# Kernel tuning notes

Measured on AMD Instinct MI355X. Metric: run time of the kernel, lower is better.

## Reference

```python
import jax, jax.numpy as jnp
import numpy as np


def setup_inputs() -> dict:
    key = jax.random.key(0)
    kq, kk, kv = jax.random.split(key, 3)
    B, H, S, D = 4, 16, 1024, 64
    Q = jax.random.normal(kq, (B, H, S, D), dtype=jnp.float32)
    K = jax.random.normal(kk, (B, H, S, D), dtype=jnp.float32)
    V = jax.random.normal(kv, (B, H, S, D), dtype=jnp.float32)
    attn_mask = jnp.ones((B, 1, 1, S), dtype=jnp.int32)  # unused by the original forward
    return {"Q": Q, "K": K, "V": V, "attn_mask": attn_mask, "d_k": D}


def reference(Q, K, V, attn_mask, d_k):
    # scores = Q @ K^T / sqrt(d_k)   -> [B, H, S, S]
    scores = jnp.einsum("bhqd,bhkd->bhqk", Q, K) / jnp.sqrt(jnp.float32(d_k))
    # attn_mask is accepted but never applied in the original module.
    p_attn = jax.nn.softmax(scores, axis=-1)
    out = jnp.einsum("bhqk,bhkd->bhqd", p_attn, V)  # [B, H, S, D]
    return (out, p_attn)
```

## Files before the change

kernel.cpp:

```cpp
#include <hip/hip_runtime.h>
#include <hip/hip_bf16.h>

#define B_N 4
#define H_N 16
#define S_N 1024
#define D_N 64
#define NELEM (B_N * H_N * S_N * D_N)

typedef __bf16 bf16;
typedef bf16  bf16x4 __attribute__((ext_vector_type(4)));
typedef bf16  bf16x8 __attribute__((ext_vector_type(8)));
typedef float f32x4  __attribute__((ext_vector_type(4)));
typedef unsigned int u32x2 __attribute__((ext_vector_type(2)));

#define AS1 __attribute__((address_space(1)))
#define AS3 __attribute__((address_space(3)))
#define GLL16(gp, lp) __builtin_amdgcn_global_load_lds((const AS1 void*)(gp), (AS3 void*)(lp), 16, 0, 0)

__global__ __launch_bounds__(256)
void prep_kv(const float* __restrict__ K, const float* __restrict__ V,
             bf16* __restrict__ Kb, bf16* __restrict__ Vt)
{
    const int b = blockIdx.x;
    if (b < 2048) {
        int t = b * 256 + threadIdx.x;
        int row = t >> 3, sub = t & 7;
        const float* src = K + (size_t)row * 64 + sub * 8;
        float4 f0 = *(const float4*)src;
        float4 f1 = *(const float4*)(src + 4);
        bf16x8 o;
        o[0] = (bf16)f0.x; o[1] = (bf16)f0.y; o[2] = (bf16)f0.z; o[3] = (bf16)f0.w;
        o[4] = (bf16)f1.x; o[5] = (bf16)f1.y; o[6] = (bf16)f1.z; o[7] = (bf16)f1.w;
        int slot = sub ^ (row & 7);
        *(bf16x8*)(Kb + (size_t)row * 64 + slot * 8) = o;
    } else {
        int wid  = (b - 2048) * 4 + (threadIdx.x >> 6);
        int lane = threadIdx.x & 63;
        int bh = wid >> 7, chunk = wid & 127;
        const float* src = V + (size_t)bh * S_N * D_N + (size_t)chunk * 8 * 64 + lane;
        bf16x8 o;
#pragma unroll
        for (int j = 0; j < 8; ++j) o[j] = (bf16)src[j * 64];
        int slot = (chunk & 7) ^ (lane & 7);
        bf16* dst = Vt + (size_t)bh * D_N * S_N + (size_t)lane * S_N
                       + (chunk >> 3) * 64 + slot * 8;
        *(bf16x8*)dst = o;
    }
}

__global__ __launch_bounds__(256)
void sdpa_main(const float* __restrict__ Qf, const bf16* __restrict__ Kb,
               const bf16* __restrict__ Vt, float* __restrict__ Og,
               float* __restrict__ Pg)
{
    __shared__ __attribute__((aligned(128))) bf16 K_lds[2][4096];
    __shared__ __attribute__((aligned(128))) bf16 V_lds[2][4096];
    __shared__ __attribute__((aligned(128))) bf16 Pt_lds[4][1024];

    const int bid = blockIdx.x;
    const int swz = (bid & 7) * 128 + (bid >> 3);
    const int bh = swz >> 4, qtile = swz & 15;

    const int tid = threadIdx.x;
    const int wave = tid >> 6, lane = tid & 63;
    const int l16 = lane & 15, lgrp = lane >> 4;
    const int swx = (l16 & 7) << 4;

    const float* Qp = Qf + (size_t)bh * S_N * D_N;
    const bf16* Kp = Kb + (size_t)bh * S_N * D_N;
    const bf16* Vp = Vt + (size_t)bh * D_N * S_N;
    float* Op = Og + (size_t)bh * S_N * D_N;
    float* Pp = Pg + (size_t)bh * S_N * S_N;

    const int qrow = qtile * 64 + wave * 16 + l16;
    bf16x8 aq[2];
#pragma unroll
    for (int ds = 0; ds < 2; ++ds) {
        const float* src = Qp + (size_t)qrow * 64 + ds * 32 + lgrp * 8;
        float4 f0 = *(const float4*)src;
        float4 f1 = *(const float4*)(src + 4);
        aq[ds][0] = (bf16)(f0.x * 0.125f); aq[ds][1] = (bf16)(f0.y * 0.125f);
        aq[ds][2] = (bf16)(f0.z * 0.125f); aq[ds][3] = (bf16)(f0.w * 0.125f);
        aq[ds][4] = (bf16)(f1.x * 0.125f); aq[ds][5] = (bf16)(f1.y * 0.125f);
        aq[ds][6] = (bf16)(f1.z * 0.125f); aq[ds][7] = (bf16)(f1.w * 0.125f);
    }

    auto stage_k = [&](int kt, bf16* dst) {
        const bf16* gk = Kp + (size_t)kt * 64;
        GLL16(gk + (wave    ) * 512 + lane * 8, dst + (wave    ) * 512);
        GLL16(gk + (wave + 4) * 512 + lane * 8, dst + (wave + 4) * 512);
    };
    auto stage_k2 = [&](int kt, bf16* dst0, bf16* dst1) {
        const bf16* gk = Kp + (size_t)kt * 64;
        GLL16(gk + (wave     ) * 512 + lane * 8, dst0 + (wave    ) * 512);
        GLL16(gk + (wave + 4 ) * 512 + lane * 8, dst0 + (wave + 4) * 512);
        GLL16(gk + (wave + 8 ) * 512 + lane * 8, dst1 + (wave    ) * 512);
        GLL16(gk + (wave + 12) * 512 + lane * 8, dst1 + (wave + 4) * 512);
    };
    auto stage_v = [&](int kt, bf16* dst) {
        const int dr = lane >> 3, c7 = lane & 7;
        GLL16(Vp + (size_t)((wave    ) * 8 + dr) * S_N + kt + c7 * 8, dst + (wave    ) * 512);
        GLL16(Vp + (size_t)((wave + 4) * 8 + dr) * S_N + kt + c7 * 8, dst + (wave + 4) * 512);
    };

    auto scores = [&](const bf16* base, f32x4 (&acc)[4]) {
#pragma unroll
        for (int kb = 0; kb < 4; ++kb) {
            acc[kb] = (f32x4){0.f, 0.f, 0.f, 0.f};
#pragma unroll
            for (int ds = 0; ds < 2; ++ds) {
                bf16x8 bk = *(const bf16x8*)((const char*)base
                            + (kb * 16 + l16) * 128
                            + ((ds * 64 + lgrp * 16) ^ swx));
                acc[kb] = __builtin_amdgcn_mfma_f32_16x16x32_bf16(aq[ds], bk, acc[kb], 0, 0, 0);
            }
        }
    };

    float lsum[4] = {0.f, 0.f, 0.f, 0.f};
    stage_k2(0, &K_lds[0][0], &K_lds[1][0]);
    __syncthreads();
    for (int c = 0; c < 8; ++c) {
        const bf16* b0 = (c & 1) ? &V_lds[0][0] : &K_lds[0][0];
        const bf16* b1 = (c & 1) ? &V_lds[1][0] : &K_lds[1][0];
        bf16* n0 = (c & 1) ? &K_lds[0][0] : &V_lds[0][0];
        bf16* n1 = (c & 1) ? &K_lds[1][0] : &V_lds[1][0];
        if (c < 7) stage_k2((c + 1) * 128, n0, n1);
        f32x4 acc[4];
        scores(b0, acc);
#pragma unroll
        for (int kb = 0; kb < 4; ++kb)
#pragma unroll
            for (int r = 0; r < 4; ++r) lsum[r] += __expf(acc[kb][r]);
        scores(b1, acc);
#pragma unroll
        for (int kb = 0; kb < 4; ++kb)
#pragma unroll
            for (int r = 0; r < 4; ++r) lsum[r] += __expf(acc[kb][r]);
        __syncthreads();
    }
    float rl[4];
#pragma unroll
    for (int r = 0; r < 4; ++r) {
        float s = lsum[r];
        s += __shfl_xor(s, 1, 64);
        s += __shfl_xor(s, 2, 64);
        s += __shfl_xor(s, 4, 64);
        s += __shfl_xor(s, 8, 64);
        rl[r] = 1.0f / s;
    }

    f32x4 oacc[4];
#pragma unroll
    for (int db = 0; db < 4; ++db) oacc[db] = (f32x4){0.f, 0.f, 0.f, 0.f};

    const unsigned ptoff = (unsigned)(uintptr_t)(AS3 bf16*)(&Pt_lds[wave][0]);
    const int qg = qtile * 64 + wave * 16 + l16;

    stage_k(0, &K_lds[0][0]);
    stage_v(0, &V_lds[0][0]);
    __syncthreads();
    for (int t = 0; t < 16; ++t) {
        const int kt = t * 64, buf = t & 1;

        f32x4 acc[4];
        scores(&K_lds[buf][0], acc);

        if (t < 15) {
            stage_k(kt + 64, &K_lds[buf ^ 1][0]);
            stage_v(kt + 64, &V_lds[buf ^ 1][0]);
        }

#pragma unroll
        for (int kb = 0; kb < 4; ++kb) {
            bf16x4 pk;
#pragma unroll
            for (int r = 0; r < 4; ++r) pk[r] = (bf16)(__expf(acc[kb][r]) * rl[r]);
            *(bf16x4*)((char*)&Pt_lds[wave][0] + (kb * 16 + l16) * 32 + lgrp * 8) = pk;
        }
        asm volatile("s_waitcnt lgkmcnt(0)" ::: "memory");

        const bf16* vb = &V_lds[buf][0];
#pragma unroll
        for (int ks = 0; ks < 2; ++ks) {
            bf16x8 bv0 = *(const bf16x8*)((const char*)vb + (l16     ) * 128 + ((ks * 64 + lgrp * 16) ^ swx));
            bf16x8 bv1 = *(const bf16x8*)((const char*)vb + (16 + l16) * 128 + ((ks * 64 + lgrp * 16) ^ swx));
            bf16x8 bv2 = *(const bf16x8*)((const char*)vb + (32 + l16) * 128 + ((ks * 64 + lgrp * 16) ^ swx));
            bf16x8 bv3 = *(const bf16x8*)((const char*)vb + (48 + l16) * 128 + ((ks * 64 + lgrp * 16) ^ swx));

            u32x2 t0, t1;
            unsigned a = ptoff + ks * 1024 + lgrp * 256 + l16 * 8;
            asm volatile("ds_read_b64_tr_b16 %0, %2\n\t"
                         "ds_read_b64_tr_b16 %1, %2 offset:128"
                         : "=&v"(t0), "=&v"(t1) : "v"(a));
            asm volatile("s_waitcnt lgkmcnt(0)" ::: "memory");
            __builtin_amdgcn_sched_barrier(0);

            bf16x8 ap;
            ((unsigned*)&ap)[0] = t0[0]; ((unsigned*)&ap)[1] = t0[1];
            ((unsigned*)&ap)[2] = t1[0]; ((unsigned*)&ap)[3] = t1[1];

            float4 o0, o1;
            o0.x = __uint_as_float(t0[0] << 16);
            o0.y = __uint_as_float(t0[0] & 0xffff0000u);
            o0.z = __uint_as_float(t0[1] << 16);
            o0.w = __uint_as_float(t0[1] & 0xffff0000u);
            o1.x = __uint_as_float(t1[0] << 16);
            o1.y = __uint_as_float(t1[0] & 0xffff0000u);
            o1.z = __uint_as_float(t1[1] << 16);
            o1.w = __uint_as_float(t1[1] & 0xffff0000u);
            float* pp = Pp + (size_t)qg * S_N + kt + ks * 32 + lgrp * 8;
            *(float4*)pp = o0;
            *(float4*)(pp + 4) = o1;

            oacc[0] = __builtin_amdgcn_mfma_f32_16x16x32_bf16(ap, bv0, oacc[0], 0, 0, 0);
            oacc[1] = __builtin_amdgcn_mfma_f32_16x16x32_bf16(ap, bv1, oacc[1], 0, 0, 0);
            oacc[2] = __builtin_amdgcn_mfma_f32_16x16x32_bf16(ap, bv2, oacc[2], 0, 0, 0);
            oacc[3] = __builtin_amdgcn_mfma_f32_16x16x32_bf16(ap, bv3, oacc[3], 0, 0, 0);
        }
        __syncthreads();
    }

    const int qb0 = qtile * 64 + wave * 16 + lgrp * 4;
#pragma unroll
    for (int db = 0; db < 4; ++db)
#pragma unroll
        for (int r = 0; r < 4; ++r)
            Op[(size_t)(qb0 + r) * D_N + db * 16 + l16] = oacc[db][r];
}

__global__ __launch_bounds__(256)
void sdpa_fused(const float* __restrict__ Qg, const float* __restrict__ Kg,
                const float* __restrict__ Vg, float* __restrict__ Og,
                float* __restrict__ Pg)
{
    constexpr int LDP = 72;
    __shared__ bf16 K_lds [64][LDP];
    __shared__ bf16 Vt_lds[64][LDP];
    __shared__ bf16 P_lds [4][16][LDP];

    const int qtile = blockIdx.x;
    const int bh    = blockIdx.y;
    const int tid   = threadIdx.x;
    const int wave  = tid >> 6;
    const int lane  = tid & 63;
    const int l16   = lane & 15;
    const int lgrp  = lane >> 4;

    const float* Qp = Qg + (size_t)bh * S_N * D_N;
    const float* Kp = Kg + (size_t)bh * S_N * D_N;
    const float* Vp = Vg + (size_t)bh * S_N * D_N;
    float* Op = Og + (size_t)bh * S_N * D_N;
    float* Pp = Pg + (size_t)bh * S_N * S_N;

    const int qrow = qtile * 64 + wave * 16 + l16;
    bf16x8 aq[2];
#pragma unroll
    for (int ds = 0; ds < 2; ++ds) {
        const float* src = Qp + qrow * D_N + ds * 32 + lgrp * 8;
        float4 f0 = *(const float4*)(src);
        float4 f1 = *(const float4*)(src + 4);
        aq[ds][0] = (bf16)(f0.x * 0.125f); aq[ds][1] = (bf16)(f0.y * 0.125f);
        aq[ds][2] = (bf16)(f0.z * 0.125f); aq[ds][3] = (bf16)(f0.w * 0.125f);
        aq[ds][4] = (bf16)(f1.x * 0.125f); aq[ds][5] = (bf16)(f1.y * 0.125f);
        aq[ds][6] = (bf16)(f1.z * 0.125f); aq[ds][7] = (bf16)(f1.w * 0.125f);
    }

    auto stage_k = [&](int kt) {
#pragma unroll
        for (int i = 0; i < 4; ++i) {
            int slot = tid + i * 256;
            int row = slot >> 4, c4 = slot & 15;
            float4 f = *(const float4*)(Kp + (kt + row) * D_N + c4 * 4);
            bf16x4 pk = {(bf16)f.x, (bf16)f.y, (bf16)f.z, (bf16)f.w};
            *(bf16x4*)&K_lds[row][c4 * 4] = pk;
        }
    };
    auto stage_v = [&](int kt) {
#pragma unroll
        for (int i = 0; i < 4; ++i) {
            int slot = tid + i * 256;
            int row = slot >> 4, c4 = slot & 15;
            float4 f = *(const float4*)(Vp + (kt + row) * D_N + c4 * 4);
            Vt_lds[c4 * 4 + 0][row] = (bf16)f.x;
            Vt_lds[c4 * 4 + 1][row] = (bf16)f.y;
            Vt_lds[c4 * 4 + 2][row] = (bf16)f.z;
            Vt_lds[c4 * 4 + 3][row] = (bf16)f.w;
        }
    };
    auto compute_scores = [&](f32x4 (&acc)[4]) {
#pragma unroll
        for (int kb = 0; kb < 4; ++kb) {
            acc[kb] = (f32x4){0.f, 0.f, 0.f, 0.f};
#pragma unroll
            for (int ds = 0; ds < 2; ++ds) {
                bf16x8 bk = *(const bf16x8*)&K_lds[kb * 16 + l16][ds * 32 + lgrp * 8];
                acc[kb] = __builtin_amdgcn_mfma_f32_16x16x32_bf16(aq[ds], bk, acc[kb], 0, 0, 0);
            }
        }
    };

    float lsum[4] = {0.f, 0.f, 0.f, 0.f};
    for (int kt = 0; kt < S_N; kt += 64) {
        __syncthreads();
        stage_k(kt);
        __syncthreads();
        f32x4 acc[4];
        compute_scores(acc);
#pragma unroll
        for (int kb = 0; kb < 4; ++kb)
#pragma unroll
            for (int r = 0; r < 4; ++r) lsum[r] += __expf(acc[kb][r]);
    }
    float rl[4];
#pragma unroll
    for (int r = 0; r < 4; ++r) {
        float s = lsum[r];
        s += __shfl_xor(s, 1, 64);
        s += __shfl_xor(s, 2, 64);
        s += __shfl_xor(s, 4, 64);
        s += __shfl_xor(s, 8, 64);
        rl[r] = 1.0f / s;
    }

    f32x4 oacc[4];
#pragma unroll
    for (int db = 0; db < 4; ++db) oacc[db] = (f32x4){0.f, 0.f, 0.f, 0.f};
    const int qb0 = qtile * 64 + wave * 16 + lgrp * 4;

    for (int kt = 0; kt < S_N; kt += 64) {
        __syncthreads();
        stage_k(kt);
        stage_v(kt);
        __syncthreads();

        f32x4 acc[4];
        compute_scores(acc);
#pragma unroll
        for (int kb = 0; kb < 4; ++kb) {
#pragma unroll
            for (int r = 0; r < 4; ++r) {
                float p = __expf(acc[kb][r]) * rl[r];
                Pp[(size_t)(qb0 + r) * S_N + (kt + kb * 16 + l16)] = p;
                P_lds[wave][lgrp * 4 + r][kb * 16 + l16] = (bf16)p;
            }
        }
#pragma unroll
        for (int ks = 0; ks < 2; ++ks) {
            bf16x8 ap = *(const bf16x8*)&P_lds[wave][l16][ks * 32 + lgrp * 8];
#pragma unroll
            for (int db = 0; db < 4; ++db) {
                bf16x8 bv = *(const bf16x8*)&Vt_lds[db * 16 + l16][ks * 32 + lgrp * 8];
                oacc[db] = __builtin_amdgcn_mfma_f32_16x16x32_bf16(ap, bv, oacc[db], 0, 0, 0);
            }
        }
    }

#pragma unroll
    for (int db = 0; db < 4; ++db)
#pragma unroll
        for (int r = 0; r < 4; ++r)
            Op[(size_t)(qb0 + r) * D_N + db * 16 + l16] = oacc[db][r];
}

extern "C" void kernel_launch(void* const* d_in, const int* in_sizes, int n_in,
                              void* d_out, int out_size, void* d_ws, size_t ws_size,
                              hipStream_t stream) {
    const float* Q = (const float*)d_in[0];
    const float* K = (const float*)d_in[1];
    const float* V = (const float*)d_in[2];
    float* Out = (float*)d_out;
    float* P   = (float*)d_out + (size_t)NELEM;

    const size_t need = (size_t)NELEM * 2 * 2;
    if (ws_size >= need) {
        bf16* Kb = (bf16*)d_ws;
        bf16* Vt = Kb + NELEM;
        prep_kv<<<dim3(4096), dim3(256), 0, stream>>>(K, V, Kb, Vt);
        sdpa_main<<<dim3(1024), dim3(256), 0, stream>>>(Q, Kb, Vt, Out, P);
    } else {
        sdpa_fused<<<dim3(16, 64), dim3(256), 0, stream>>>(Q, K, V, Out, P);
    }
}
```

Before: 96.24 us.

## Cache unnormalized bf16 exp scores in registers to skip second QK^T pass

The first pass now keeps exp(scores) as bf16 in a register array, 64 bf16x4 values per thread, while accumulating row sums. The second pass then only rescales these cached values and streams V, instead of recomputing QK^T and exp from K in LDS. This removes half the MFMA score work and the second round of K loads, but adds heavy register pressure that can lower occupancy or cause spills. It also adds double rounding to bf16 (exp, then normalized P), which changes precision slightly.

```diff
diff --git a/kernel.cpp b/kernel.cpp
--- a/kernel.cpp
+++ b/kernel.cpp
@@ -90,13 +90,6 @@
         GLL16(gk + (wave    ) * 512 + lane * 8, dst + (wave    ) * 512);
         GLL16(gk + (wave + 4) * 512 + lane * 8, dst + (wave + 4) * 512);
     };
-    auto stage_k2 = [&](int kt, bf16* dst0, bf16* dst1) {
-        const bf16* gk = Kp + (size_t)kt * 64;
-        GLL16(gk + (wave     ) * 512 + lane * 8, dst0 + (wave    ) * 512);
-        GLL16(gk + (wave + 4 ) * 512 + lane * 8, dst0 + (wave + 4) * 512);
-        GLL16(gk + (wave + 8 ) * 512 + lane * 8, dst1 + (wave    ) * 512);
-        GLL16(gk + (wave + 12) * 512 + lane * 8, dst1 + (wave + 4) * 512);
-    };
     auto stage_v = [&](int kt, bf16* dst) {
         const int dr = lane >> 3, c7 = lane & 7;
         GLL16(Vp + (size_t)((wave    ) * 8 + dr) * S_N + kt + c7 * 8, dst + (wave    ) * 512);
@@ -117,26 +110,29 @@
         }
     };
 
+    bf16x4 pc[16][4];
+
     float lsum[4] = {0.f, 0.f, 0.f, 0.f};
-    stage_k2(0, &K_lds[0][0], &K_lds[1][0]);
+    stage_k(0, &K_lds[0][0]);
     __syncthreads();
-    for (int c = 0; c < 8; ++c) {
-        const bf16* b0 = (c & 1) ? &V_lds[0][0] : &K_lds[0][0];
-        const bf16* b1 = (c & 1) ? &V_lds[1][0] : &K_lds[1][0];
-        bf16* n0 = (c & 1) ? &K_lds[0][0] : &V_lds[0][0];
-        bf16* n1 = (c & 1) ? &K_lds[1][0] : &V_lds[1][0];
-        if (c < 7) stage_k2((c + 1) * 128, n0, n1);
+#pragma unroll
+    for (int t = 0; t < 16; ++t) {
+        const int buf = t & 1;
+        if (t < 15) stage_k((t + 1) * 64, &K_lds[buf ^ 1][0]);
+        if (t == 15) stage_v(0, &V_lds[0][0]);
         f32x4 acc[4];
-        scores(b0, acc);
-#pragma unroll
-        for (int kb = 0; kb < 4; ++kb)
-#pragma unroll
-            for (int r = 0; r < 4; ++r) lsum[r] += __expf(acc[kb][r]);
-        scores(b1, acc);
-#pragma unroll
-        for (int kb = 0; kb < 4; ++kb)
-#pragma unroll
-            for (int r = 0; r < 4; ++r) lsum[r] += __expf(acc[kb][r]);
+        scores(&K_lds[buf][0], acc);
+#pragma unroll
+        for (int kb = 0; kb < 4; ++kb) {
+            bf16x4 pk;
+#pragma unroll
+            for (int r = 0; r < 4; ++r) {
+                float e = __expf(acc[kb][r]);
+                lsum[r] += e;
+                pk[r] = (bf16)e;
+            }
+            pc[t][kb] = pk;
+        }
         __syncthreads();
     }
     float rl[4];
@@ -157,25 +153,17 @@
     const unsigned ptoff = (unsigned)(uintptr_t)(AS3 bf16*)(&Pt_lds[wave][0]);
     const int qg = qtile * 64 + wave * 16 + l16;
 
-    stage_k(0, &K_lds[0][0]);
-    stage_v(0, &V_lds[0][0]);
-    __syncthreads();
+#pragma unroll
     for (int t = 0; t < 16; ++t) {
         const int kt = t * 64, buf = t & 1;
-
-        f32x4 acc[4];
-        scores(&K_lds[buf][0], acc);
-
-        if (t < 15) {
-            stage_k(kt + 64, &K_lds[buf ^ 1][0]);
-            stage_v(kt + 64, &V_lds[buf ^ 1][0]);
-        }
+        if (t < 15) stage_v(kt + 64, &V_lds[buf ^ 1][0]);
 
 #pragma unroll
         for (int kb = 0; kb < 4; ++kb) {
             bf16x4 pk;
 #pragma unroll
-            for (int r = 0; r < 4; ++r) pk[r] = (bf16)(__expf(acc[kb][r]) * rl[r]);
+            for (int r = 0; r < 4; ++r)
+                pk[r] = (bf16)((float)pc[t][kb][r] * rl[r]);
             *(bf16x4*)((char*)&Pt_lds[wave][0] + (kb * 16 + l16) * 32 + lgrp * 8) = pk;
         }
         asm volatile("s_waitcnt lgkmcnt(0)" ::: "memory");
```

Result: slower. 132.4 us (+37.6%).
